# Performance work log

Measured on AMD Instinct MI355X. Metric: run time of the kernel, lower is better.

The kernel has to match this reference:

```python
import jax, jax.numpy as jnp
import numpy as np

N_A, N_P, E = 50000, 50000, 600000
H, D = 8, 16
C = H * D  # hidden_channels = 128
OUT = 16
F_A, F_P = 256, 128
NEG_SLOPE = 0.2
EPS = 1e-5


def setup_inputs():
    key = jax.random.key(0)
    ks = jax.random.split(key, 16)
    return {
        'x_author': jax.random.normal(ks[0], (N_A, F_A), jnp.float32),
        'x_paper': jax.random.normal(ks[1], (N_P, F_P), jnp.float32),
        'W_a': jax.random.normal(ks[2], (F_A, C), jnp.float32) / np.sqrt(F_A).astype(np.float32),
        'b_a': jnp.zeros((C,), jnp.float32),
        'W_p': jax.random.normal(ks[3], (F_P, C), jnp.float32) / np.sqrt(F_P).astype(np.float32),
        'b_p': jnp.zeros((C,), jnp.float32),
        'att_src_ap': jax.random.normal(ks[4], (H, D), jnp.float32) * 0.1,
        'att_dst_ap': jax.random.normal(ks[5], (H, D), jnp.float32) * 0.1,
        'att_src_pp': jax.random.normal(ks[6], (H, D), jnp.float32) * 0.1,
        'att_dst_pp': jax.random.normal(ks[7], (H, D), jnp.float32) * 0.1,
        'k_W': jax.random.normal(ks[8], (C, C), jnp.float32) / np.sqrt(C).astype(np.float32),
        'k_b': jnp.zeros((C,), jnp.float32),
        'q': jax.random.normal(ks[9], (C,), jnp.float32) * 0.1,
        'norm_w': jnp.ones((C,), jnp.float32),
        'norm_b': jnp.zeros((C,), jnp.float32),
        'norm_ms': jnp.ones((C,), jnp.float32),
        'lin_W': jax.random.normal(ks[10], (C, OUT), jnp.float32) / np.sqrt(C).astype(np.float32),
        'lin_b': jnp.zeros((OUT,), jnp.float32),
        'edge_ap': jax.random.randint(ks[11], (2, E), 0, N_A),
        'edge_pp': jax.random.randint(ks[12], (2, E), 0, N_P),
    }


def _edge_type_out(h_src, h_dst, edge, a_src, a_dst, n_dst):
    # Node-level attention for one edge type (PyG HANConv per-metapath GAT).
    alpha_s = jnp.einsum('nhd,hd->nh', h_src, a_src)  # [N_src, H]
    alpha_d = jnp.einsum('nhd,hd->nh', h_dst, a_dst)  # [N_dst, H]
    src, dst = edge[0], edge[1]
    alpha = alpha_s[src] + alpha_d[dst]                       # [E, H]
    alpha = jnp.where(alpha >= 0, alpha, NEG_SLOPE * alpha)   # leaky_relu(0.2)
    m = jax.ops.segment_max(alpha, dst, num_segments=n_dst)
    e = jnp.exp(alpha - m[dst])
    denom = jax.ops.segment_sum(e, dst, num_segments=n_dst)
    attn = e / denom[dst]                                     # softmax over incoming edges
    msg = h_src[src] * attn[:, :, None]                       # [E, H, D]
    out = jax.ops.segment_sum(msg, dst, num_segments=n_dst)   # [n_dst, H, D]
    return jax.nn.relu(out.reshape(n_dst, H * D))


def reference(x_author, x_paper, W_a, b_a, W_p, b_p, att_src_ap, att_dst_ap,
              att_src_pp, att_dst_pp, k_W, k_b, q, norm_w, norm_b, norm_ms,
              lin_W, lin_b, edge_ap, edge_pp):
    # per-node-type projections -> [N, H, D]
    h_a = (x_author @ W_a + b_a).reshape(N_A, H, D)
    h_p = (x_paper @ W_p + b_p).reshape(N_P, H, D)
    # per-edge-type node-level attention + aggregation (both target 'paper')
    out_ap = _edge_type_out(h_a, h_p, edge_ap, att_src_ap, att_dst_ap, N_P)
    out_pp = _edge_type_out(h_p, h_p, edge_pp, att_src_pp, att_dst_pp, N_P)
    # semantic-level attention across the R=2 meta-paths
    outs = jnp.stack([out_ap, out_pp], axis=0)               # [R, N_P, C]
    w = jnp.tanh(outs @ k_W + k_b).mean(axis=1) @ q          # [R]
    beta = jax.nn.softmax(w)
    out = jnp.einsum('rnc,r->nc', outs, beta)                # [N_P, C]
    # GraphNorm (single graph: stats over all nodes)
    mean = out.mean(axis=0)
    o = out - mean * norm_ms
    var = (o * o).mean(axis=0)
    o = norm_w * o / jnp.sqrt(var + EPS) + norm_b
    # final classifier
    return o @ lin_W + lin_b
```

## Files before the change

kernel.cpp:

```cpp
#include <hip/hip_runtime.h>
#include <math.h>

#define NN   50000
#define EE   600000
#define CCH  128
#define HH   8
#define DD   16
#define OUTC 16
#define NEG  0.2f
#define EPSN 1e-5f
#define SCHUNKS 586
#define CAP 64
#define SBKT 32

typedef _Float16 f16x8 __attribute__((ext_vector_type(8)));
typedef float    f32x4 __attribute__((ext_vector_type(4)));

__device__ __forceinline__ float fast_tanh(float x) {
    x = fminf(10.f, fmaxf(-10.f, x));
    float e = __expf(2.f * x);
    return (e - 1.f) / (e + 1.f);
}

__device__ __forceinline__ float lrelu(float x) {
    return (x >= 0.f) ? x : NEG * x;
}

__global__ __launch_bounds__(256) void convw_k(const float* __restrict__ W_a,
        const float* __restrict__ W_p, const float* __restrict__ k_W,
        const float* __restrict__ lin_W, _Float16* __restrict__ Wt_a,
        _Float16* __restrict__ Wt_p, _Float16* __restrict__ kWt,
        _Float16* __restrict__ linWt)
{
    int id = blockIdx.x * 256 + threadIdx.x;
    if (id < 32768) {
        int k = id >> 7, n = id & 127;
        Wt_a[n * 256 + k] = (_Float16)W_a[id];
    } else if (id < 49152) {
        int i = id - 32768; int k = i >> 7, n = i & 127;
        Wt_p[n * 128 + k] = (_Float16)W_p[i];
    } else if (id < 65536) {
        int i = id - 49152; int k = i >> 7, n = i & 127;
        kWt[n * 128 + k] = (_Float16)k_W[i];
    } else if (id < 67584) {
        int i = id - 65536; int k = i >> 4, n = i & 15;
        linWt[n * 128 + k] = (_Float16)lin_W[i];
    }
}

__global__ __launch_bounds__(256) void gemm2h_k(const float* __restrict__ X_a,
        const float* __restrict__ X_p, const _Float16* __restrict__ Wt_a,
        const _Float16* __restrict__ Wt_p, const float* __restrict__ b_a,
        const float* __restrict__ b_p,
        const float* __restrict__ att_s_ap, const float* __restrict__ att_d_ap,
        const float* __restrict__ att_s_pp, const float* __restrict__ att_d_pp,
        _Float16* __restrict__ h_a, _Float16* __restrict__ h_p,
        float* __restrict__ as_ap, float* __restrict__ ad_ap,
        float* __restrict__ as_pp, float* __restrict__ ad_pp,
        const int* __restrict__ ea, const int* __restrict__ ep,
        int* __restrict__ fill, int* __restrict__ csrp, int GBn)
{
    __shared__ _Float16 As[64][40];
    __shared__ _Float16 Bs[128][40];
    const int t = threadIdx.x;
    if ((int)blockIdx.x >= 2 * GBn) {
        int bb = (int)blockIdx.x - 2 * GBn;
        int base = bb * 2048 + t;
        int d[8];
#pragma unroll
        for (int it = 0; it < 8; ++it) {
            int e = base + it * 256;
            int dd = -1;
            if (e < EE) dd = ea[EE + e];
            else if (e < 2 * EE) dd = NN + ep[e];
            d[it] = dd;
        }
#pragma unroll
        for (int it = 0; it < 8; ++it) {
            int dd = d[it];
            if (dd >= 0) {
                int e = base + it * 256;
                int pos = atomicAdd(&fill[dd], 1);
                if (pos < CAP) {
                    int s = (e < EE) ? ea[e] : ep[e - EE];
                    csrp[(size_t)dd * CAP + pos] = s;
                }
            }
        }
        return;
    }
    const int which = ((int)blockIdx.x >= GBn) ? 1 : 0;
    const float* X = which ? X_p : X_a;
    const _Float16* Wt = which ? Wt_p : Wt_a;
    const float* bias = which ? b_p : b_a;
    _Float16* Y = which ? h_p : h_a;
    const int K = which ? 128 : 256;
    const int r0 = (blockIdx.x - which * GBn) * 64;
    const int lane = t & 63;
    const int wv = t >> 6;
    const int m16 = lane & 15;
    const int kq = lane >> 4;
    f32x4 acc[8];
#pragma unroll
    for (int i = 0; i < 8; ++i) acc[i] = (f32x4){0.f, 0.f, 0.f, 0.f};

    const int ar = t >> 2;
    const int ak = (t & 3) * 8;
    const int br = t >> 1;
    const int bk = (t & 1) * 16;

    for (int kc = 0; kc < K; kc += 32) {
        int row = r0 + ar;
        f16x8 av;
        if (row < NN) {
            const float4* gp = (const float4*)&X[row * K + kc + ak];
            float4 x0 = gp[0], x1 = gp[1];
            av[0] = (_Float16)x0.x; av[1] = (_Float16)x0.y;
            av[2] = (_Float16)x0.z; av[3] = (_Float16)x0.w;
            av[4] = (_Float16)x1.x; av[5] = (_Float16)x1.y;
            av[6] = (_Float16)x1.z; av[7] = (_Float16)x1.w;
        } else {
#pragma unroll
            for (int j = 0; j < 8; ++j) av[j] = (_Float16)0.f;
        }
        *(f16x8*)&As[ar][ak] = av;
        const f16x8* wp = (const f16x8*)&Wt[br * K + kc + bk];
        *(f16x8*)&Bs[br][bk]     = wp[0];
        *(f16x8*)&Bs[br][bk + 8] = wp[1];
        __syncthreads();
        f16x8 af = *(const f16x8*)&As[wv * 16 + m16][kq * 8];
#pragma unroll
        for (int i = 0; i < 8; ++i) {
            f16x8 bf = *(const f16x8*)&Bs[i * 16 + m16][kq * 8];
            acc[i] = __builtin_amdgcn_mfma_f32_16x16x32_f16(af, bf, acc[i], 0, 0, 0);
        }
        __syncthreads();
    }
    const int rbase = r0 + wv * 16 + kq * 4;
#pragma unroll
    for (int i = 0; i < 8; ++i) {
        int col = i * 16 + m16;
        float bv = bias[col];
        float hv[4];
#pragma unroll
        for (int rr = 0; rr < 4; ++rr) hv[rr] = acc[i][rr] + bv;
#pragma unroll
        for (int rr = 0; rr < 4; ++rr)
            if (rbase + rr < NN) Y[(rbase + rr) * 128 + col] = (_Float16)hv[rr];
        if (which == 0) {
            float av = att_s_ap[i * 16 + m16];
            float p[4];
#pragma unroll
            for (int rr = 0; rr < 4; ++rr) p[rr] = hv[rr] * av;
#pragma unroll
            for (int x = 1; x < 16; x <<= 1)
#pragma unroll
                for (int rr = 0; rr < 4; ++rr) p[rr] += __shfl_xor(p[rr], x, 64);
            if (m16 == 0) {
#pragma unroll
                for (int rr = 0; rr < 4; ++rr)
                    if (rbase + rr < NN) as_ap[(rbase + rr) * 8 + i] = p[rr];
            }
        } else {
            float a1 = att_d_ap[i * 16 + m16];
            float a2 = att_s_pp[i * 16 + m16];
            float a3 = att_d_pp[i * 16 + m16];
            float p1[4], p2[4], p3[4];
#pragma unroll
            for (int rr = 0; rr < 4; ++rr) {
                p1[rr] = hv[rr] * a1; p2[rr] = hv[rr] * a2; p3[rr] = hv[rr] * a3;
            }
#pragma unroll
            for (int x = 1; x < 16; x <<= 1) {
#pragma unroll
                for (int rr = 0; rr < 4; ++rr) {
                    p1[rr] += __shfl_xor(p1[rr], x, 64);
                    p2[rr] += __shfl_xor(p2[rr], x, 64);
                    p3[rr] += __shfl_xor(p3[rr], x, 64);
                }
            }
            if (m16 == 0) {
#pragma unroll
                for (int rr = 0; rr < 4; ++rr) {
                    if (rbase + rr < NN) {
                        ad_ap[(rbase + rr) * 8 + i] = p1[rr];
                        as_pp[(rbase + rr) * 8 + i] = p2[rr];
                        ad_pp[(rbase + rr) * 8 + i] = p3[rr];
                    }
                }
            }
        }
    }
}

__global__ __launch_bounds__(256) void agg4f_k(
        const _Float16* __restrict__ h_a, const _Float16* __restrict__ h_p,
        const float* __restrict__ as_ap, const float* __restrict__ ad_ap,
        const float* __restrict__ as_pp, const float* __restrict__ ad_pp,
        const int* __restrict__ fill, const int* __restrict__ csrp,
        const _Float16* __restrict__ kWt, const float* __restrict__ kb,
        const float* __restrict__ qv,
        _Float16* __restrict__ out_ap, _Float16* __restrict__ out_pp,
        float* __restrict__ wacc, float* __restrict__ statsb)
{
    __shared__ _Float16 Aap[16][136];
    __shared__ _Float16 App[16][136];
    __shared__ float sbuf[640];
    __shared__ float wred[4];
    const int t = threadIdx.x;
    const int wave = t >> 6, lane = t & 63;
    const int q = lane >> 4, sub = lane & 15;
    const int slot = wave * 4 + q;
    const int n = blockIdx.x * 16 + slot;
    const int h = sub >> 1;
    for (int i = t; i < 640; i += 256) sbuf[i] = 0.f;

    float adva = ad_ap[n * 8 + h];
    float advp = ad_pp[n * 8 + h];
    int cnt_a = fill[n];      if (cnt_a > CAP) cnt_a = CAP;
    int cnt_p = fill[NN + n]; if (cnt_p > CAP) cnt_p = CAP;
    const int* rowA = &csrp[(size_t)n * CAP];
    const int* rowP = &csrp[(size_t)(NN + n) * CAP];
    float la = 0.f, lp = 0.f;
    float accA[8] = {0.f,0.f,0.f,0.f,0.f,0.f,0.f,0.f};
    float accP[8] = {0.f,0.f,0.f,0.f,0.f,0.f,0.f,0.f};
    int pa = 0, pb = 0;
    while (pa + 3 < cnt_a && pb + 3 < cnt_p) {
        int4 ra = *(const int4*)&rowA[pa];
        int4 rp = *(const int4*)&rowP[pb];
        float aa0 = as_ap[ra.x*8+h] + adva, aa1 = as_ap[ra.y*8+h] + adva;
        float aa2 = as_ap[ra.z*8+h] + adva, aa3 = as_ap[ra.w*8+h] + adva;
        float ap0 = as_pp[rp.x*8+h] + advp, ap1 = as_pp[rp.y*8+h] + advp;
        float ap2 = as_pp[rp.z*8+h] + advp, ap3 = as_pp[rp.w*8+h] + advp;
        float wa0 = __expf(lrelu(aa0)), wa1 = __expf(lrelu(aa1));
        float wa2 = __expf(lrelu(aa2)), wa3 = __expf(lrelu(aa3));
        float wp0 = __expf(lrelu(ap0)), wp1 = __expf(lrelu(ap1));
        float wp2 = __expf(lrelu(ap2)), wp3 = __expf(lrelu(ap3));
        f16x8 va0 = *(const f16x8*)&h_a[ra.x*CCH + sub*8];
        f16x8 va1 = *(const f16x8*)&h_a[ra.y*CCH + sub*8];
        f16x8 va2 = *(const f16x8*)&h_a[ra.z*CCH + sub*8];
        f16x8 va3 = *(const f16x8*)&h_a[ra.w*CCH + sub*8];
        f16x8 vp0 = *(const f16x8*)&h_p[rp.x*CCH + sub*8];
        f16x8 vp1 = *(const f16x8*)&h_p[rp.y*CCH + sub*8];
        f16x8 vp2 = *(const f16x8*)&h_p[rp.z*CCH + sub*8];
        f16x8 vp3 = *(const f16x8*)&h_p[rp.w*CCH + sub*8];
        la += (wa0 + wa1) + (wa2 + wa3);
        lp += (wp0 + wp1) + (wp2 + wp3);
#pragma unroll
        for (int i = 0; i < 8; ++i) {
            accA[i] += (wa0*(float)va0[i] + wa1*(float)va1[i])
                     + (wa2*(float)va2[i] + wa3*(float)va3[i]);
            accP[i] += (wp0*(float)vp0[i] + wp1*(float)vp1[i])
                     + (wp2*(float)vp2[i] + wp3*(float)vp3[i]);
        }
        pa += 4; pb += 4;
    }
    for (; pa + 3 < cnt_a; pa += 4) {
        int4 ra = *(const int4*)&rowA[pa];
        float aa0 = as_ap[ra.x*8+h] + adva, aa1 = as_ap[ra.y*8+h] + adva;
        float aa2 = as_ap[ra.z*8+h] + adva, aa3 = as_ap[ra.w*8+h] + adva;
        float wa0 = __expf(lrelu(aa0)), wa1 = __expf(lrelu(aa1));
        float wa2 = __expf(lrelu(aa2)), wa3 = __expf(lrelu(aa3));
        f16x8 va0 = *(const f16x8*)&h_a[ra.x*CCH + sub*8];
        f16x8 va1 = *(const f16x8*)&h_a[ra.y*CCH + sub*8];
        f16x8 va2 = *(const f16x8*)&h_a[ra.z*CCH + sub*8];
        f16x8 va3 = *(const f16x8*)&h_a[ra.w*CCH + sub*8];
        la += (wa0 + wa1) + (wa2 + wa3);
#pragma unroll
        for (int i = 0; i < 8; ++i)
            accA[i] += (wa0*(float)va0[i] + wa1*(float)va1[i])
                     + (wa2*(float)va2[i] + wa3*(float)va3[i]);
    }
    for (; pa < cnt_a; ++pa) {
        int s0 = rowA[pa];
        float w0 = __expf(lrelu(as_ap[s0*8+h] + adva));
        f16x8 v0 = *(const f16x8*)&h_a[s0*CCH + sub*8];
        la += w0;
#pragma unroll
        for (int i = 0; i < 8; ++i) accA[i] += w0*(float)v0[i];
    }
    for (; pb + 3 < cnt_p; pb += 4) {
        int4 rp = *(const int4*)&rowP[pb];
        float ap0 = as_pp[rp.x*8+h] + advp, ap1 = as_pp[rp.y*8+h] + advp;
        float ap2 = as_pp[rp.z*8+h] + advp, ap3 = as_pp[rp.w*8+h] + advp;
        float wp0 = __expf(lrelu(ap0)), wp1 = __expf(lrelu(ap1));
        float wp2 = __expf(lrelu(ap2)), wp3 = __expf(lrelu(ap3));
        f16x8 vp0 = *(const f16x8*)&h_p[rp.x*CCH + sub*8];
        f16x8 vp1 = *(const f16x8*)&h_p[rp.y*CCH + sub*8];
        f16x8 vp2 = *(const f16x8*)&h_p[rp.z*CCH + sub*8];
        f16x8 vp3 = *(const f16x8*)&h_p[rp.w*CCH + sub*8];
        lp += (wp0 + wp1) + (wp2 + wp3);
#pragma unroll
        for (int i = 0; i < 8; ++i)
            accP[i] += (wp0*(float)vp0[i] + wp1*(float)vp1[i])
                     + (wp2*(float)vp2[i] + wp3*(float)vp3[i]);
    }
    for (; pb < cnt_p; ++pb) {
        int s0 = rowP[pb];
        float w0 = __expf(lrelu(as_pp[s0*8+h] + advp));
        f16x8 v0 = *(const f16x8*)&h_p[s0*CCH + sub*8];
        lp += w0;
#pragma unroll
        for (int i = 0; i < 8; ++i) accP[i] += w0*(float)v0[i];
    }
    float inva = (la > 0.f) ? 1.f/la : 0.f;
    float invp = (lp > 0.f) ? 1.f/lp : 0.f;
    float oa[8], ob[8];
#pragma unroll
    for (int i = 0; i < 8; ++i) {
        oa[i] = fmaxf(accA[i]*inva, 0.f);
        ob[i] = fmaxf(accP[i]*invp, 0.f);
    }
    f16x8 va, vb;
#pragma unroll
    for (int i = 0; i < 8; ++i) { va[i] = (_Float16)oa[i]; vb[i] = (_Float16)ob[i]; }
    *(f16x8*)&out_ap[n * CCH + sub * 8] = va;
    *(f16x8*)&out_pp[n * CCH + sub * 8] = vb;
    *(f16x8*)&Aap[slot][sub * 8] = va;
    *(f16x8*)&App[slot][sub * 8] = vb;
    float sa[8], sb[8], ssa[8], ssb[8], sab[8];
#pragma unroll
    for (int j = 0; j < 8; ++j) {
        float a = oa[j], bq = ob[j];
        sa[j] = a; sb[j] = bq; ssa[j] = a*a; ssb[j] = bq*bq; sab[j] = a*bq;
    }
#pragma unroll
    for (int x = 16; x < 64; x <<= 1) {
#pragma unroll
        for (int j = 0; j < 8; ++j) {
            sa[j]  += __shfl_xor(sa[j],  x, 64);
            sb[j]  += __shfl_xor(sb[j],  x, 64);
            ssa[j] += __shfl_xor(ssa[j], x, 64);
            ssb[j] += __shfl_xor(ssb[j], x, 64);
            sab[j] += __shfl_xor(sab[j], x, 64);
        }
    }
    __syncthreads();
    if (lane < 16) {
        int c0 = sub * 8;
#pragma unroll
        for (int j = 0; j < 8; ++j) {
            atomicAdd(&sbuf[c0 + j],       sa[j]);
            atomicAdd(&sbuf[128 + c0 + j], sb[j]);
            atomicAdd(&sbuf[256 + c0 + j], ssa[j]);
            atomicAdd(&sbuf[384 + c0 + j], ssb[j]);
            atomicAdd(&sbuf[512 + c0 + j], sab[j]);
        }
    }
    const int m16 = lane & 15, kq = lane >> 4;
    const int path = wave >> 1;
    float local = 0.f;
#pragma unroll
    for (int j = 0; j < 4; ++j) {
        int ct = (wave & 1) * 4 + j;
        f32x4 acc2 = (f32x4){0.f, 0.f, 0.f, 0.f};
#pragma unroll
        for (int kc = 0; kc < 128; kc += 32) {
            f16x8 af = path ? *(const f16x8*)&App[m16][kc + kq * 8]
                            : *(const f16x8*)&Aap[m16][kc + kq * 8];
            f16x8 bf = *(const f16x8*)&kWt[(ct * 16 + m16) * 128 + kc + kq * 8];
            acc2 = __builtin_amdgcn_mfma_f32_16x16x32_f16(af, bf, acc2, 0, 0, 0);
        }
        float kbc = kb[ct * 16 + m16], qc = qv[ct * 16 + m16];
#pragma unroll
        for (int rr = 0; rr < 4; ++rr)
            local += fast_tanh(acc2[rr] + kbc) * qc;
    }
#pragma unroll
    for (int x = 1; x < 64; x <<= 1) local += __shfl_xor(local, x, 64);
    if (lane == 0) wred[wave] = local;
    __syncthreads();
    if (t == 0) atomicAdd(&wacc[(blockIdx.x & 15) * 16],       wred[0] + wred[1]);
    if (t == 1) atomicAdd(&wacc[256 + (blockIdx.x & 15) * 16], wred[2] + wred[3]);
    if (t < 128) {
        float* sp = statsb + (size_t)(blockIdx.x & (SBKT - 1)) * 128;
        atomicAdd(&sp[t],                sbuf[t]);
        atomicAdd(&sp[SBKT*128 + t],     sbuf[128 + t]);
        atomicAdd(&sp[2*SBKT*128 + t],   sbuf[256 + t]);
        atomicAdd(&sp[3*SBKT*128 + t],   sbuf[384 + t]);
        atomicAdd(&sp[4*SBKT*128 + t],   sbuf[512 + t]);
    }
}

__global__ __launch_bounds__(256) void final2_k(
        const _Float16* __restrict__ oa, const _Float16* __restrict__ ob,
        const float* __restrict__ wacc, const float* __restrict__ statsb,
        const float* __restrict__ ms, const float* __restrict__ nw,
        const float* __restrict__ nb,
        const _Float16* __restrict__ linWt, const float* __restrict__ linb,
        float* __restrict__ out)
{
    __shared__ _Float16 As[64][136];
    __shared__ float scl[128], shf[128];
    __shared__ float bcoef[2];
    int t = threadIdx.x;
    if (t < 128) {
        float w0s = 0.f, w1s = 0.f;
#pragma unroll
        for (int i = 0; i < 16; ++i) {
            w0s += wacc[i * 16];
            w1s += wacc[256 + i * 16];
        }
        float w0 = w0s * (1.f / NN), w1 = w1s * (1.f / NN);
        float mm = fmaxf(w0, w1);
        float e0 = __expf(w0 - mm), e1 = __expf(w1 - mm);
        float b0 = e0 / (e0 + e1), b1 = e1 / (e0 + e1);
        if (t == 0) { bcoef[0] = b0; bcoef[1] = b1; }
        int c = t;
        float vsA = 0.f, vsB = 0.f, vssA = 0.f, vssB = 0.f, vsAB = 0.f;
        for (int i = 0; i < SBKT; ++i) {
            vsA  += statsb[i * 128 + c];
            vsB  += statsb[SBKT*128 + i * 128 + c];
            vssA += statsb[2*SBKT*128 + i * 128 + c];
            vssB += statsb[3*SBKT*128 + i * 128 + c];
            vsAB += statsb[4*SBKT*128 + i * 128 + c];
        }
        float mean = (b0 * vsA + b1 * vsB) * (1.f / NN);
        float ex2 = (b0 * b0 * vssA + 2.f * b0 * b1 * vsAB + b1 * b1 * vssB) * (1.f / NN);
        float a = mean * ms[c];
        float var = ex2 - 2.f * a * mean + a * a;
        float sc = nw[c] * rsqrtf(var + EPSN);
        scl[c] = sc;
        shf[c] = nb[c] - a * sc;
    }
    __syncthreads();
    float b0 = bcoef[0], b1 = bcoef[1];
    int r0 = blockIdx.x * 64;
    int row = t >> 2, cp = (t & 3) * 32;
    int gr = r0 + row;
    if (gr < NN) {
#pragma unroll
        for (int i = 0; i < 4; ++i) {
            int c0 = cp + i * 8;
            f16x8 va = *(const f16x8*)&oa[gr * CCH + c0];
            f16x8 vb = *(const f16x8*)&ob[gr * CCH + c0];
            f16x8 o;
#pragma unroll
            for (int e2 = 0; e2 < 8; ++e2) {
                float v = b0 * (float)va[e2] + b1 * (float)vb[e2];
                o[e2] = (_Float16)(v * scl[c0 + e2] + shf[c0 + e2]);
            }
            *(f16x8*)&As[row][c0] = o;
        }
    } else {
        f16x8 z;
#pragma unroll
        for (int e2 = 0; e2 < 8; ++e2) z[e2] = (_Float16)0.f;
#pragma unroll
        for (int i = 0; i < 4; ++i) *(f16x8*)&As[row][cp + i * 8] = z;
    }
    __syncthreads();
    int lane = t & 63, wv = t >> 6;
    int m16 = lane & 15, kq = lane >> 4;
    f32x4 acc = (f32x4){0.f, 0.f, 0.f, 0.f};
#pragma unroll
    for (int kc = 0; kc < 128; kc += 32) {
        f16x8 af = *(const f16x8*)&As[wv * 16 + m16][kc + kq * 8];
        f16x8 bf = *(const f16x8*)&linWt[m16 * 128 + kc + kq * 8];
        acc = __builtin_amdgcn_mfma_f32_16x16x32_f16(af, bf, acc, 0, 0, 0);
    }
    float lb = linb[m16];
#pragma unroll
    for (int r = 0; r < 4; ++r) {
        int gr2 = r0 + wv * 16 + kq * 4 + r;
        if (gr2 < NN) out[gr2 * 16 + m16] = acc[r] + lb;
    }
}

extern "C" void kernel_launch(void* const* d_in, const int* in_sizes, int n_in,
                              void* d_out, int out_size, void* d_ws, size_t ws_size,
                              hipStream_t stream) {
    const float* x_a   = (const float*)d_in[0];
    const float* x_p   = (const float*)d_in[1];
    const float* W_a   = (const float*)d_in[2];
    const float* b_a   = (const float*)d_in[3];
    const float* W_p   = (const float*)d_in[4];
    const float* b_p   = (const float*)d_in[5];
    const float* att_src_ap = (const float*)d_in[6];
    const float* att_dst_ap = (const float*)d_in[7];
    const float* att_src_pp = (const float*)d_in[8];
    const float* att_dst_pp = (const float*)d_in[9];
    const float* k_W   = (const float*)d_in[10];
    const float* k_b   = (const float*)d_in[11];
    const float* q     = (const float*)d_in[12];
    const float* norm_w = (const float*)d_in[13];
    const float* norm_b = (const float*)d_in[14];
    const float* norm_ms = (const float*)d_in[15];
    const float* lin_W = (const float*)d_in[16];
    const float* lin_b = (const float*)d_in[17];
    const int* edge_ap = (const int*)d_in[18];
    const int* edge_pp = (const int*)d_in[19];
    float* out = (float*)d_out;

    char* base = (char*)d_ws;
    size_t off = 0;
    auto alloc = [&](size_t bytes) -> void* {
        void* r = base + off;
        off += (bytes + 255) & ~(size_t)255;
        return r;
    };
    _Float16* h_a    = (_Float16*)alloc((size_t)NN * CCH * 2);
    _Float16* h_p    = (_Float16*)alloc((size_t)NN * CCH * 2);
    _Float16* out_ap = (_Float16*)alloc((size_t)NN * CCH * 2);
    _Float16* out_pp = (_Float16*)alloc((size_t)NN * CCH * 2);
    float* as_ap  = (float*)alloc((size_t)NN * HH * 4);
    float* ad_ap  = (float*)alloc((size_t)NN * HH * 4);
    float* as_pp  = (float*)alloc((size_t)NN * HH * 4);
    float* ad_pp  = (float*)alloc((size_t)NN * HH * 4);
    _Float16* Wt_a = (_Float16*)alloc((size_t)128 * 256 * 2);
    _Float16* Wt_p = (_Float16*)alloc((size_t)128 * 128 * 2);
    _Float16* kWt  = (_Float16*)alloc((size_t)128 * 128 * 2);
    _Float16* linWt = (_Float16*)alloc((size_t)16 * 128 * 2);
    int* csrp = (int*)alloc((size_t)2 * NN * CAP * 4);
    const size_t ZCOUNT = 100000 + 512 + 5 * SBKT * 128;
    int* zz = (int*)alloc(ZCOUNT * 4);
    int* fill   = zz;
    float* wacc = (float*)(zz + 100000);
    float* statsb = (float*)(zz + 100512);

    (void)in_sizes; (void)n_in; (void)out_size; (void)ws_size;

    hipMemsetAsync(zz, 0, ZCOUNT * 4, stream);

    convw_k<<<264, 256, 0, stream>>>(W_a, W_p, k_W, lin_W, Wt_a, Wt_p, kWt, linWt);

    const int GB = (NN + 63) / 64;
    gemm2h_k<<<2 * GB + SCHUNKS, 256, 0, stream>>>(
        x_a, x_p, Wt_a, Wt_p, b_a, b_p,
        att_src_ap, att_dst_ap, att_src_pp, att_dst_pp,
        h_a, h_p, as_ap, ad_ap, as_pp, ad_pp,
        edge_ap, edge_pp, fill, csrp, GB);

    agg4f_k<<<NN / 16, 256, 0, stream>>>(h_a, h_p, as_ap, ad_ap, as_pp, ad_pp,
                                         fill, csrp, kWt, k_b, q,
                                         out_ap, out_pp, wacc, statsb);

    final2_k<<<GB, 256, 0, stream>>>(out_ap, out_pp, wacc, statsb,
                                     norm_ms, norm_w, norm_b, linWt, lin_b, out);
}
```

Baseline: 372.9 us.

## Batch neighbor gathers in fixed 16/24-wide unrolled chunks and halve CSR-build block size

Replaces the 4-wide interleaved aggregation loops with a helper that issues 16 (then 8 more) independent attention and feature gathers up front, masking missing neighbours to index 0. This raises memory-level parallelism for the typical degree of about 12. It always gathers 16 rows even for low-degree nodes and uses more registers. Separately, the CSR-fill blocks now handle 1024 edges each instead of 2048, doubling the number of those blocks to spread the atomics across more blocks.

Measured after the change: 334.0 us. 10.5% less time.

```diff
diff --git a/kernel.cpp b/kernel.cpp
--- a/kernel.cpp
+++ b/kernel.cpp
@@ -9,7 +9,7 @@
 #define OUTC 16
 #define NEG  0.2f
 #define EPSN 1e-5f
-#define SCHUNKS 586
+#define SCHUNKS 1172
 #define CAP 64
 #define SBKT 32
 
@@ -65,10 +65,10 @@
     const int t = threadIdx.x;
     if ((int)blockIdx.x >= 2 * GBn) {
         int bb = (int)blockIdx.x - 2 * GBn;
-        int base = bb * 2048 + t;
-        int d[8];
-#pragma unroll
-        for (int it = 0; it < 8; ++it) {
+        int base = bb * 1024 + t;
+        int d[4];
+#pragma unroll
+        for (int it = 0; it < 4; ++it) {
             int e = base + it * 256;
             int dd = -1;
             if (e < EE) dd = ea[EE + e];
@@ -76,7 +76,7 @@
             d[it] = dd;
         }
 #pragma unroll
-        for (int it = 0; it < 8; ++it) {
+        for (int it = 0; it < 4; ++it) {
             int dd = d[it];
             if (dd >= 0) {
                 int e = base + it * 256;
@@ -189,6 +189,64 @@
                     }
                 }
             }
+        }
+    }
+}
+
+__device__ __forceinline__ void agg_path(
+        const _Float16* __restrict__ hsrc, const float* __restrict__ as,
+        float adv, int cnt, const int* __restrict__ row, int h, int sub,
+        float* acc, float& l)
+{
+    int4 r0 = *(const int4*)&row[0];
+    int4 r1 = *(const int4*)&row[4];
+    int4 r2 = *(const int4*)&row[8];
+    int4 r3 = *(const int4*)&row[12];
+    int s[16] = {r0.x, r0.y, r0.z, r0.w, r1.x, r1.y, r1.z, r1.w,
+                 r2.x, r2.y, r2.z, r2.w, r3.x, r3.y, r3.z, r3.w};
+#pragma unroll
+    for (int e = 0; e < 16; ++e) s[e] = (e < cnt) ? s[e] : 0;
+    float av[16];
+#pragma unroll
+    for (int e = 0; e < 16; ++e) av[e] = as[s[e] * 8 + h];
+    f16x8 hv[16];
+#pragma unroll
+    for (int e = 0; e < 16; ++e)
+        hv[e] = *(const f16x8*)&hsrc[(size_t)s[e] * CCH + sub * 8];
+#pragma unroll
+    for (int e = 0; e < 16; ++e) {
+        float w = (e < cnt) ? __expf(lrelu(av[e] + adv)) : 0.f;
+        l += w;
+#pragma unroll
+        for (int i = 0; i < 8; ++i) acc[i] += w * (float)hv[e][i];
+    }
+    if (cnt > 16) {
+        int4 r4 = *(const int4*)&row[16];
+        int4 r5 = *(const int4*)&row[20];
+        int s2[8] = {r4.x, r4.y, r4.z, r4.w, r5.x, r5.y, r5.z, r5.w};
+#pragma unroll
+        for (int e = 0; e < 8; ++e) s2[e] = (16 + e < cnt) ? s2[e] : 0;
+        float av2[8];
+#pragma unroll
+        for (int e = 0; e < 8; ++e) av2[e] = as[s2[e] * 8 + h];
+        f16x8 hv2[8];
+#pragma unroll
+        for (int e = 0; e < 8; ++e)
+            hv2[e] = *(const f16x8*)&hsrc[(size_t)s2[e] * CCH + sub * 8];
+#pragma unroll
+        for (int e = 0; e < 8; ++e) {
+            float w = (16 + e < cnt) ? __expf(lrelu(av2[e] + adv)) : 0.f;
+            l += w;
+#pragma unroll
+            for (int i = 0; i < 8; ++i) acc[i] += w * (float)hv2[e][i];
+        }
+        for (int p = 24; p < cnt; ++p) {
+            int s0 = row[p];
+            float w = __expf(lrelu(as[s0 * 8 + h] + adv));
+            f16x8 v = *(const f16x8*)&hsrc[(size_t)s0 * CCH + sub * 8];
+            l += w;
+#pragma unroll
+            for (int i = 0; i < 8; ++i) acc[i] += w * (float)v[i];
         }
     }
 }
@@ -219,90 +277,13 @@
     float advp = ad_pp[n * 8 + h];
     int cnt_a = fill[n];      if (cnt_a > CAP) cnt_a = CAP;
     int cnt_p = fill[NN + n]; if (cnt_p > CAP) cnt_p = CAP;
-    const int* rowA = &csrp[(size_t)n * CAP];
-    const int* rowP = &csrp[(size_t)(NN + n) * CAP];
     float la = 0.f, lp = 0.f;
     float accA[8] = {0.f,0.f,0.f,0.f,0.f,0.f,0.f,0.f};
     float accP[8] = {0.f,0.f,0.f,0.f,0.f,0.f,0.f,0.f};
-    int pa = 0, pb = 0;
-    while (pa + 3 < cnt_a && pb + 3 < cnt_p) {
-        int4 ra = *(const int4*)&rowA[pa];
-        int4 rp = *(const int4*)&rowP[pb];
-        float aa0 = as_ap[ra.x*8+h] + adva, aa1 = as_ap[ra.y*8+h] + adva;
-        float aa2 = as_ap[ra.z*8+h] + adva, aa3 = as_ap[ra.w*8+h] + adva;
-        float ap0 = as_pp[rp.x*8+h] + advp, ap1 = as_pp[rp.y*8+h] + advp;
-        float ap2 = as_pp[rp.z*8+h] + advp, ap3 = as_pp[rp.w*8+h] + advp;
-        float wa0 = __expf(lrelu(aa0)), wa1 = __expf(lrelu(aa1));
-        float wa2 = __expf(lrelu(aa2)), wa3 = __expf(lrelu(aa3));
-        float wp0 = __expf(lrelu(ap0)), wp1 = __expf(lrelu(ap1));
-        float wp2 = __expf(lrelu(ap2)), wp3 = __expf(lrelu(ap3));
-        f16x8 va0 = *(const f16x8*)&h_a[ra.x*CCH + sub*8];
-        f16x8 va1 = *(const f16x8*)&h_a[ra.y*CCH + sub*8];
-        f16x8 va2 = *(const f16x8*)&h_a[ra.z*CCH + sub*8];
-        f16x8 va3 = *(const f16x8*)&h_a[ra.w*CCH + sub*8];
-        f16x8 vp0 = *(const f16x8*)&h_p[rp.x*CCH + sub*8];
-        f16x8 vp1 = *(const f16x8*)&h_p[rp.y*CCH + sub*8];
-        f16x8 vp2 = *(const f16x8*)&h_p[rp.z*CCH + sub*8];
-        f16x8 vp3 = *(const f16x8*)&h_p[rp.w*CCH + sub*8];
-        la += (wa0 + wa1) + (wa2 + wa3);
-        lp += (wp0 + wp1) + (wp2 + wp3);
-#pragma unroll
-        for (int i = 0; i < 8; ++i) {
-            accA[i] += (wa0*(float)va0[i] + wa1*(float)va1[i])
-                     + (wa2*(float)va2[i] + wa3*(float)va3[i]);
-            accP[i] += (wp0*(float)vp0[i] + wp1*(float)vp1[i])
-                     + (wp2*(float)vp2[i] + wp3*(float)vp3[i]);
-        }
-        pa += 4; pb += 4;
-    }
-    for (; pa + 3 < cnt_a; pa += 4) {
-        int4 ra = *(const int4*)&rowA[pa];
-        float aa0 = as_ap[ra.x*8+h] + adva, aa1 = as_ap[ra.y*8+h] + adva;
-        float aa2 = as_ap[ra.z*8+h] + adva, aa3 = as_ap[ra.w*8+h] + adva;
-        float wa0 = __expf(lrelu(aa0)), wa1 = __expf(lrelu(aa1));
-        float wa2 = __expf(lrelu(aa2)), wa3 = __expf(lrelu(aa3));
-        f16x8 va0 = *(const f16x8*)&h_a[ra.x*CCH + sub*8];
-        f16x8 va1 = *(const f16x8*)&h_a[ra.y*CCH + sub*8];
-        f16x8 va2 = *(const f16x8*)&h_a[ra.z*CCH + sub*8];
-        f16x8 va3 = *(const f16x8*)&h_a[ra.w*CCH + sub*8];
-        la += (wa0 + wa1) + (wa2 + wa3);
-#pragma unroll
-        for (int i = 0; i < 8; ++i)
-            accA[i] += (wa0*(float)va0[i] + wa1*(float)va1[i])
-                     + (wa2*(float)va2[i] + wa3*(float)va3[i]);
-    }
-    for (; pa < cnt_a; ++pa) {
-        int s0 = rowA[pa];
-        float w0 = __expf(lrelu(as_ap[s0*8+h] + adva));
-        f16x8 v0 = *(const f16x8*)&h_a[s0*CCH + sub*8];
-        la += w0;
-#pragma unroll
-        for (int i = 0; i < 8; ++i) accA[i] += w0*(float)v0[i];
-    }
-    for (; pb + 3 < cnt_p; pb += 4) {
-        int4 rp = *(const int4*)&rowP[pb];
-        float ap0 = as_pp[rp.x*8+h] + advp, ap1 = as_pp[rp.y*8+h] + advp;
-        float ap2 = as_pp[rp.z*8+h] + advp, ap3 = as_pp[rp.w*8+h] + advp;
-        float wp0 = __expf(lrelu(ap0)), wp1 = __expf(lrelu(ap1));
-        float wp2 = __expf(lrelu(ap2)), wp3 = __expf(lrelu(ap3));
-        f16x8 vp0 = *(const f16x8*)&h_p[rp.x*CCH + sub*8];
-        f16x8 vp1 = *(const f16x8*)&h_p[rp.y*CCH + sub*8];
-        f16x8 vp2 = *(const f16x8*)&h_p[rp.z*CCH + sub*8];
-        f16x8 vp3 = *(const f16x8*)&h_p[rp.w*CCH + sub*8];
-        lp += (wp0 + wp1) + (wp2 + wp3);
-#pragma unroll
-        for (int i = 0; i < 8; ++i)
-            accP[i] += (wp0*(float)vp0[i] + wp1*(float)vp1[i])
-                     + (wp2*(float)vp2[i] + wp3*(float)vp3[i]);
-    }
-    for (; pb < cnt_p; ++pb) {
-        int s0 = rowP[pb];
-        float w0 = __expf(lrelu(as_pp[s0*8+h] + advp));
-        f16x8 v0 = *(const f16x8*)&h_p[s0*CCH + sub*8];
-        lp += w0;
-#pragma unroll
-        for (int i = 0; i < 8; ++i) accP[i] += w0*(float)v0[i];
-    }
+
+    agg_path(h_a, as_ap, adva, cnt_a, &csrp[(size_t)n * CAP],        h, sub, accA, la);
+    agg_path(h_p, as_pp, advp, cnt_p, &csrp[(size_t)(NN + n) * CAP], h, sub, accP, lp);
+
     float inva = (la > 0.f) ? 1.f/la : 0.f;
     float invp = (lp > 0.f) ? 1.f/lp : 0.f;
     float oa[8], ob[8];
```
